# Optimization experiments

Measured on AMD Instinct MI355X. Metric: run time of the kernel, lower is better.

## Reference

```python
import jax, jax.numpy as jnp
import numpy as np

N_NODES = 163842
SEQ_LEN = 9
IN_CH = 32
OUT_CH = 64


def setup_inputs() -> dict:
    key = jax.random.key(0)
    k1, k2, k3 = jax.random.split(key, 3)
    x = jax.random.normal(k1, (N_NODES, IN_CH), dtype=jnp.float32)
    indices = jax.random.randint(k2, (N_NODES, SEQ_LEN), 0, N_NODES, dtype=jnp.int64)
    # xavier_uniform for Linear(IN_CH*SEQ_LEN, OUT_CH)
    fan_in = IN_CH * SEQ_LEN
    limit = float(np.sqrt(6.0 / (fan_in + OUT_CH)))
    W = jax.random.uniform(k3, (OUT_CH, fan_in), dtype=jnp.float32, minval=-limit, maxval=limit)
    b = jnp.zeros((OUT_CH,), dtype=jnp.float32)
    return {"x": x, "indices": indices, "W": W, "b": b}


def reference(x, indices, W, b):
    # gather spiral neighbor features: [n_nodes, seq_len, in_ch]
    gathered = x[indices]
    # flatten to [n_nodes, seq_len*in_ch] and apply Linear (y = g @ W^T + b)
    g = gathered.reshape(indices.shape[0], -1)
    return jnp.einsum("nf,of->no", g, W) + b
```

## Files before the change

### kernel.cpp

```cpp
#include <hip/hip_runtime.h>
#include <hip/hip_bf16.h>


constexpr int NN   = 163842;
constexpr int SEQ  = 9;
constexpr int INC  = 32;
constexpr int OUTC = 64;
constexpr int FAN  = SEQ * INC;
constexpr int NTILES = (NN + 63) / 64;
constexpr int TPB  = 6;
constexpr int WELEM = SEQ * 4 * OUTC * 8;

using s8    = __attribute__((ext_vector_type(8))) short;
using f32x4 = __attribute__((ext_vector_type(4))) float;

__device__ __forceinline__ unsigned f2bf(float f) {
    union { float f; unsigned u; } c; c.f = f;
    unsigned u = c.u;
    u += 0x7fffu + ((u >> 16) & 1u);
    return (u >> 16) & 0xffffu;
}

__global__ __launch_bounds__(256) void convert_pack_kernel(
    const float* __restrict__ x, const float* __restrict__ W,
    unsigned short* __restrict__ xb, unsigned short* __restrict__ wpk)
{
    const int xq = NN * INC / 4;
    int t = blockIdx.x * blockDim.x + threadIdx.x;
    if (t < xq) {
        float4 v = reinterpret_cast<const float4*>(x)[t];
        unsigned lo = f2bf(v.x) | (f2bf(v.y) << 16);
        unsigned hi = f2bf(v.z) | (f2bf(v.w) << 16);
        reinterpret_cast<uint2*>(xb)[t] = make_uint2(lo, hi);
    } else if (t < xq + WELEM / 4) {
        int j4 = t - xq;
        int c4 = j4 & 1, o = (j4 >> 1) & 63, k4 = (j4 >> 7) & 3, s = j4 >> 9;
        float4 v = *reinterpret_cast<const float4*>(
            W + (size_t)o * FAN + s * INC + k4 * 8 + c4 * 4);
        unsigned lo = f2bf(v.x) | (f2bf(v.y) << 16);
        unsigned hi = f2bf(v.z) | (f2bf(v.w) << 16);
        reinterpret_cast<uint2*>(wpk)[j4] = make_uint2(lo, hi);
    }
}

__global__ __launch_bounds__(256) void spiral_gemm_kernel(
    const int* __restrict__ idx,
    const unsigned short* __restrict__ xb,
    const unsigned short* __restrict__ wpk,
    const float* __restrict__ bias,
    float* __restrict__ out)
{
    __shared__ unsigned short wlds[WELEM];

    const int tid  = threadIdx.x;
    const int lane = tid & 63;
    const int wid  = tid >> 6;
    const int lc   = lane & 15;
    const int lk   = lane >> 4;
    const int kb   = lk * 8;

    {
        const uint4* s4 = reinterpret_cast<const uint4*>(wpk);
        uint4* d4 = reinterpret_cast<uint4*>(wlds);
        #pragma unroll
        for (int k = 0; k < 9; ++k) d4[tid + k * 256] = s4[tid + k * 256];
    }

    f32x4 b4[4];
    #pragma unroll
    for (int f = 0; f < 4; ++f)
        b4[f] = *reinterpret_cast<const f32x4*>(bias + f * 16 + lk * 4);

    __syncthreads();

    const int t0    = blockIdx.x * TPB;
    const int lastT = min(t0 + TPB, NTILES) - 1;

    int iA[SEQ], iB[SEQ];
    s8  fA[SEQ], fB[SEQ];

    auto loadIdx = [&](int t, int (&iv)[SEQ]) {
        const int node = min(t * 64 + wid * 16 + lc, NN - 1);
        const int* ip = idx + (size_t)node * SEQ;
        #pragma unroll
        for (int s = 0; s < SEQ; ++s) iv[s] = ip[s];
    };
    auto gath = [&](const int (&iv)[SEQ], s8 (&xf)[SEQ]) {
        #pragma unroll
        for (int s = 0; s < SEQ; ++s)
            xf[s] = *reinterpret_cast<const s8*>(xb + (size_t)iv[s] * INC + kb);
    };
    auto computeStore = [&](int t, const s8 (&xf)[SEQ]) {
        f32x4 acc[4] = {};
        #pragma unroll
        for (int s = 0; s < SEQ; ++s) {
            #pragma unroll
            for (int f = 0; f < 4; ++f) {
                s8 wf = *reinterpret_cast<const s8*>(
                    &wlds[(((s * 4 + lk) * 64) + (f * 16 + lc)) * 8]);
                acc[f] = __builtin_amdgcn_mfma_f32_16x16x32_bf16(wf, xf[s], acc[f], 0, 0, 0);
            }
        }
        const int node = t * 64 + wid * 16 + lc;
        if (node < NN) {
            #pragma unroll
            for (int f = 0; f < 4; ++f) {
                f32x4 v = acc[f] + b4[f];
                *reinterpret_cast<f32x4*>(out + (size_t)node * OUTC + f * 16 + lk * 4) = v;
            }
        }
    };

    loadIdx(t0, iA);
    gath(iA, fA);
    if (t0 + 1 <= lastT) loadIdx(t0 + 1, iB);

    #pragma unroll
    for (int k = 0; k < TPB; k += 2) {
        const int tB = t0 + k + 1, tA2 = t0 + k + 2, tB2 = t0 + k + 3;
        if (tB  <= lastT) gath(iB, fB);
        if (tA2 <= lastT) loadIdx(tA2, iA);
        computeStore(t0 + k, fA);
        if (tA2 <= lastT) gath(iA, fA);
        if (tB2 <= lastT) loadIdx(tB2, iB);
        if (tB  <= lastT) computeStore(tB, fB);
    }
}

extern "C" void kernel_launch(void* const* d_in, const int* in_sizes, int n_in,
                              void* d_out, int out_size, void* d_ws, size_t ws_size,
                              hipStream_t stream) {
    const float* x    = (const float*)d_in[0];
    const int*   idx  = (const int*)d_in[1];
    const float* W    = (const float*)d_in[2];
    const float* b    = (const float*)d_in[3];
    float*       out  = (float*)d_out;

    unsigned short* xb  = (unsigned short*)d_ws;
    unsigned short* wpk = xb + (size_t)NN * INC;

    const int ctot = NN * INC / 4 + WELEM / 4;
    convert_pack_kernel<<<(ctot + 255) / 256, 256, 0, stream>>>(x, W, xb, wpk);

    const int nblocks = (NTILES + TPB - 1) / TPB;
    spiral_gemm_kernel<<<nblocks, 256, 0, stream>>>(idx, xb, wpk, b, out);
}
```

Before: 42.87 us.

## Replace multi-tile software pipeline with one tile per 512-thread block

```diff
diff --git a/kernel.cpp b/kernel.cpp
--- a/kernel.cpp
+++ b/kernel.cpp
@@ -7,8 +7,6 @@
 constexpr int INC  = 32;
 constexpr int OUTC = 64;
 constexpr int FAN  = SEQ * INC;
-constexpr int NTILES = (NN + 63) / 64;
-constexpr int TPB  = 6;
 constexpr int WELEM = SEQ * 4 * OUTC * 8;
 
 using s8    = __attribute__((ext_vector_type(8))) short;
@@ -43,7 +41,7 @@
     }
 }
 
-__global__ __launch_bounds__(256) void spiral_gemm_kernel(
+__global__ __launch_bounds__(512, 6) void spiral_gemm_kernel(
     const int* __restrict__ idx,
     const unsigned short* __restrict__ xb,
     const unsigned short* __restrict__ wpk,
@@ -63,67 +61,45 @@
         const uint4* s4 = reinterpret_cast<const uint4*>(wpk);
         uint4* d4 = reinterpret_cast<uint4*>(wlds);
         #pragma unroll
-        for (int k = 0; k < 9; ++k) d4[tid + k * 256] = s4[tid + k * 256];
+        for (int k = 0; k < 5; ++k) {
+            int i = tid + k * 512;
+            if (i < WELEM / 8) d4[i] = s4[i];
+        }
     }
 
-    f32x4 b4[4];
+    const int node = blockIdx.x * 128 + wid * 16 + lc;
+    const int nd   = min(node, NN - 1);
+    const int* ip  = idx + (size_t)nd * SEQ;
+
+    int iv[SEQ];
     #pragma unroll
-    for (int f = 0; f < 4; ++f)
-        b4[f] = *reinterpret_cast<const f32x4*>(bias + f * 16 + lk * 4);
+    for (int s = 0; s < SEQ; ++s) iv[s] = ip[s];
+
+    s8 xf[SEQ];
+    #pragma unroll
+    for (int s = 0; s < SEQ; ++s)
+        xf[s] = *reinterpret_cast<const s8*>(xb + (size_t)iv[s] * INC + kb);
 
     __syncthreads();
 
-    const int t0    = blockIdx.x * TPB;
-    const int lastT = min(t0 + TPB, NTILES) - 1;
+    f32x4 acc[4] = {};
+    #pragma unroll
+    for (int s = 0; s < SEQ; ++s) {
+        #pragma unroll
+        for (int f = 0; f < 4; ++f) {
+            s8 wf = *reinterpret_cast<const s8*>(
+                &wlds[(((s * 4 + lk) * 64) + (f * 16 + lc)) * 8]);
+            acc[f] = __builtin_amdgcn_mfma_f32_16x16x32_bf16(wf, xf[s], acc[f], 0, 0, 0);
+        }
+    }
 
-    int iA[SEQ], iB[SEQ];
-    s8  fA[SEQ], fB[SEQ];
-
-    auto loadIdx = [&](int t, int (&iv)[SEQ]) {
-        const int node = min(t * 64 + wid * 16 + lc, NN - 1);
-        const int* ip = idx + (size_t)node * SEQ;
+    if (node < NN) {
         #pragma unroll
-        for (int s = 0; s < SEQ; ++s) iv[s] = ip[s];
-    };
-    auto gath = [&](const int (&iv)[SEQ], s8 (&xf)[SEQ]) {
-        #pragma unroll
-        for (int s = 0; s < SEQ; ++s)
-            xf[s] = *reinterpret_cast<const s8*>(xb + (size_t)iv[s] * INC + kb);
-    };
-    auto computeStore = [&](int t, const s8 (&xf)[SEQ]) {
-        f32x4 acc[4] = {};
-        #pragma unroll
-        for (int s = 0; s < SEQ; ++s) {
-            #pragma unroll
-            for (int f = 0; f < 4; ++f) {
-                s8 wf = *reinterpret_cast<const s8*>(
-                    &wlds[(((s * 4 + lk) * 64) + (f * 16 + lc)) * 8]);
-                acc[f] = __builtin_amdgcn_mfma_f32_16x16x32_bf16(wf, xf[s], acc[f], 0, 0, 0);
-            }
+        for (int f = 0; f < 4; ++f) {
+            f32x4 b4 = *reinterpret_cast<const f32x4*>(bias + f * 16 + lk * 4);
+            f32x4 v = acc[f] + b4;
+            *reinterpret_cast<f32x4*>(out + (size_t)node * OUTC + f * 16 + lk * 4) = v;
         }
-        const int node = t * 64 + wid * 16 + lc;
-        if (node < NN) {
-            #pragma unroll
-            for (int f = 0; f < 4; ++f) {
-                f32x4 v = acc[f] + b4[f];
-                *reinterpret_cast<f32x4*>(out + (size_t)node * OUTC + f * 16 + lk * 4) = v;
-            }
-        }
-    };
-
-    loadIdx(t0, iA);
-    gath(iA, fA);
-    if (t0 + 1 <= lastT) loadIdx(t0 + 1, iB);
-
-    #pragma unroll
-    for (int k = 0; k < TPB; k += 2) {
-        const int tB = t0 + k + 1, tA2 = t0 + k + 2, tB2 = t0 + k + 3;
-        if (tB  <= lastT) gath(iB, fB);
-        if (tA2 <= lastT) loadIdx(tA2, iA);
-        computeStore(t0 + k, fA);
-        if (tA2 <= lastT) gath(iA, fA);
-        if (tB2 <= lastT) loadIdx(tB2, iB);
-        if (tB  <= lastT) computeStore(tB, fB);
     }
 }
 
@@ -142,6 +118,6 @@
     const int ctot = NN * INC / 4 + WELEM / 4;
     convert_pack_kernel<<<(ctot + 255) / 256, 256, 0, stream>>>(x, W, xb, wpk);
 
-    const int nblocks = (NTILES + TPB - 1) / TPB;
-    spiral_gemm_kernel<<<nblocks, 256, 0, stream>>>(idx, xb, wpk, b, out);
+    const int nblocks = (NN + 127) / 128;
+    spiral_gemm_kernel<<<nblocks, 512, 0, stream>>>(idx, xb, wpk, b, out);
 }
```

Measured after the change: 42.79 us. No clear change (-0.2%).
